# Performance work log

Hardware: AMD Instinct MI355X
Metric: run time of the kernel (lower is better)

The kernel has to match this reference:

```python
import jax, jax.numpy as jnp
import numpy as np

N_NODES = 50000
N_EDGES = 600000
IN_DIM = 64
HID = 128
LN_EPS = 1e-5


def setup_inputs() -> dict:
    key = jax.random.key(0)
    ks = jax.random.split(key, 10)
    x = jax.random.normal(ks[0], (N_NODES, IN_DIM), dtype=jnp.float32)
    edge_index = jax.random.randint(ks[1], (2, N_EDGES), 0, N_NODES, dtype=jnp.int64)
    def lin(k, fan_in, fan_out):
        bound = 1.0 / np.sqrt(fan_in)
        kw, kb = jax.random.split(k)
        W = jax.random.uniform(kw, (fan_in, fan_out), minval=-bound, maxval=bound, dtype=jnp.float32)
        b = jax.random.uniform(kb, (fan_out,), minval=-bound, maxval=bound, dtype=jnp.float32)
        return W, b
    W1, b1 = lin(ks[2], IN_DIM, HID)
    W2, b2 = lin(ks[3], HID, HID)
    W3, b3 = lin(ks[4], HID, HID)
    g1 = jnp.ones((HID,), jnp.float32); be1 = jnp.zeros((HID,), jnp.float32)
    g2 = jnp.ones((HID,), jnp.float32); be2 = jnp.zeros((HID,), jnp.float32)
    g3 = jnp.ones((HID,), jnp.float32); be3 = jnp.zeros((HID,), jnp.float32)
    return dict(x=x, edge_index=edge_index, W1=W1, b1=b1, W2=W2, b2=b2, W3=W3, b3=b3,
                g1=g1, be1=be1, g2=g2, be2=be2, g3=g3, be3=be3)


def _gnn_layer(h, W, b, src, dst, inv_cnt, g, be):
    # linear transform then mean aggregation over {neighbors ∪ self} (self-loops in src/dst)
    h = h @ W + b                                   # [N, HID]
    s = jax.ops.segment_sum(h[src], dst, num_segments=N_NODES)  # gather + scatter-sum
    h = s * inv_cnt                                 # mean aggregation
    h = jax.nn.relu(h)
    mu = jnp.mean(h, axis=-1, keepdims=True)
    var = jnp.var(h, axis=-1, keepdims=True)
    return g * (h - mu) * jax.lax.rsqrt(var + LN_EPS) + be


def reference(x, edge_index, W1, b1, W2, b2, W3, b3, g1, be1, g2, be2, g3, be3):
    loops = jnp.arange(N_NODES, dtype=edge_index.dtype)
    src = jnp.concatenate([edge_index[0], loops])   # message source (x_j)
    dst = jnp.concatenate([edge_index[1], loops])   # aggregation target
    cnt = jax.ops.segment_sum(jnp.ones_like(dst, dtype=x.dtype), dst, num_segments=N_NODES)
    inv_cnt = (1.0 / cnt)[:, None]                  # cnt >= 1 due to self loops
    h = _gnn_layer(x, W1, b1, src, dst, inv_cnt, g1, be1)
    h = _gnn_layer(h, W2, b2, src, dst, inv_cnt, g2, be2)
    h = _gnn_layer(h, W3, b3, src, dst, inv_cnt, g3, be3)
    return h
```

## Files before the change

### kernel.cpp

```cpp
#include <hip/hip_runtime.h>
#include <hip/hip_bf16.h>

#define N_NODES 50000
#define N_EDGES 600000
#define HID 128
#define LN_EPS 1e-5f

#define SCAN_BLOCK 1024
#define SCAN_NBLK ((N_NODES + SCAN_BLOCK - 1) / SCAN_BLOCK)

typedef __attribute__((ext_vector_type(8))) short bf16x8;
typedef __attribute__((ext_vector_type(4))) float f32x4;

static __device__ __forceinline__ unsigned short f2bf(float f) {
    union { float f; unsigned u; } v; v.f = f;
    unsigned u = v.u;
    u += 0x7fffu + ((u >> 16) & 1u);
    return (unsigned short)(u >> 16);
}
static __device__ __forceinline__ float bflo(unsigned u) {
    union { unsigned u; float f; } c; c.u = u << 16; return c.f;
}
static __device__ __forceinline__ float bfhi(unsigned u) {
    union { unsigned u; float f; } c; c.u = u & 0xffff0000u; return c.f;
}

__global__ __launch_bounds__(256) void count_kernel(const int* __restrict__ ei,
                                                    int* __restrict__ deg, int E) {
    int i = blockIdx.x * blockDim.x + threadIdx.x;
    if (i < E) atomicAdd(&deg[ei[E + i]], 1);
}

__global__ __launch_bounds__(SCAN_BLOCK) void deg_partial_kernel(const int* __restrict__ deg,
                                                                 int* __restrict__ partials, int n) {
    int t = threadIdx.x;
    int i = blockIdx.x * SCAN_BLOCK + t;
    int v = (i < n) ? deg[i] : 0;
    int s = v;
#pragma unroll
    for (int off = 1; off < 64; off <<= 1) s += __shfl_xor(s, off);
    __shared__ int ws[SCAN_BLOCK / 64];
    if ((t & 63) == 0) ws[t >> 6] = s;
    __syncthreads();
    if (t == 0) {
        int tot = 0;
#pragma unroll
        for (int w = 0; w < SCAN_BLOCK / 64; ++w) tot += ws[w];
        partials[blockIdx.x] = tot;
    }
}

__global__ __launch_bounds__(64) void scan_partials_kernel(int* __restrict__ partials,
                                                           int* __restrict__ row_ptr, int nblk) {
    int lane = threadIdx.x;
    int v = (lane < nblk) ? partials[lane] : 0;
    int incl = v;
#pragma unroll
    for (int off = 1; off < 64; off <<= 1) {
        int x = __shfl_up(incl, off);
        if (lane >= off) incl += x;
    }
    if (lane < nblk) partials[lane] = incl - v;
    if (lane == 63) row_ptr[N_NODES] = incl;
}

__global__ __launch_bounds__(SCAN_BLOCK) void scan_final_kernel(const int* __restrict__ deg,
                                                                const int* __restrict__ partials,
                                                                int* __restrict__ row_ptr,
                                                                int* __restrict__ cursor,
                                                                float* __restrict__ inv_cnt, int n) {
    int t = threadIdx.x;
    int i = blockIdx.x * SCAN_BLOCK + t;
    int v = (i < n) ? deg[i] : 0;
    int lane = t & 63, wid = t >> 6;
    int incl = v;
#pragma unroll
    for (int off = 1; off < 64; off <<= 1) {
        int x = __shfl_up(incl, off);
        if (lane >= off) incl += x;
    }
    __shared__ int ws[SCAN_BLOCK / 64];
    if (lane == 63) ws[wid] = incl;
    __syncthreads();
    int woff = 0;
    for (int w = 0; w < wid; ++w) woff += ws[w];
    int excl = partials[blockIdx.x] + woff + (incl - v);
    if (i < n) {
        row_ptr[i] = excl;
        cursor[i]  = excl;
        inv_cnt[i] = 1.0f / (float)(v + 1);
    }
}

__global__ __launch_bounds__(256) void fill_kernel(const int* __restrict__ ei,
                                                   int* __restrict__ cursor,
                                                   int* __restrict__ col, int E) {
    int i = blockIdx.x * blockDim.x + threadIdx.x;
    if (i < E) {
        int s = ei[i];
        int d = ei[E + i];
        int p = atomicAdd(&cursor[d], 1);
        col[p] = s;
    }
}

__global__ __launch_bounds__(256) void cast_x_kernel(const float* __restrict__ x,
                                                     unsigned short* __restrict__ xb, int n8) {
    int i = blockIdx.x * 256 + threadIdx.x;
    if (i < n8) {
        float4 a = ((const float4*)x)[i * 2];
        float4 b = ((const float4*)x)[i * 2 + 1];
        int4 o;
        o.x = (int)f2bf(a.x) | ((int)f2bf(a.y) << 16);
        o.y = (int)f2bf(a.z) | ((int)f2bf(a.w) << 16);
        o.z = (int)f2bf(b.x) | ((int)f2bf(b.y) << 16);
        o.w = (int)f2bf(b.z) | ((int)f2bf(b.w) << 16);
        ((int4*)xb)[i] = o;
    }
}

__global__ __launch_bounds__(256) void wswz_kernel(const float* __restrict__ W,
                                                   unsigned short* __restrict__ dst, int K) {
    int i = blockIdx.x * 256 + threadIdx.x;
    if (i < K * 128) {
        int k = i >> 7, col = i & 127;
        dst[(((k >> 3) * 128) + col) * 8 + (k & 7)] = f2bf(W[i]);
    }
}

template <int K>
__global__ __launch_bounds__(256) void gemm_mfma_kernel(
    const unsigned short* __restrict__ A,
    const unsigned short* __restrict__ Wswz,
    const float* __restrict__ bias,
    unsigned short* __restrict__ out, int N) {
    __shared__ unsigned short Bl[K * 128];
    __shared__ float bl[128];
    int t = threadIdx.x;
    for (int i = t; i < K * 16; i += 256)
        ((int4*)Bl)[i] = ((const int4*)Wswz)[i];
    if (t < 128) bl[t] = bias[t];
    __syncthreads();

    int lane = t & 63;
    int w = t >> 6;
    int r0 = blockIdx.x * 64 + w * 16;
    int colb = lane & 15;
    int kg = lane >> 4;
    int rowa = min(r0 + colb, N - 1);

    f32x4 acc[8];
#pragma unroll
    for (int c = 0; c < 8; ++c) acc[c] = (f32x4){0.f, 0.f, 0.f, 0.f};

    const bf16x8* Blv = (const bf16x8*)Bl;
    for (int s = 0; s < K; s += 32) {
        bf16x8 afrag = *(const bf16x8*)&A[(size_t)rowa * K + s + kg * 8];
        int kb = (s >> 3) + kg;
#pragma unroll
        for (int c = 0; c < 8; ++c) {
            bf16x8 bfrag = Blv[kb * 128 + c * 16 + colb];
            acc[c] = __builtin_amdgcn_mfma_f32_16x16x32_bf16(afrag, bfrag, acc[c], 0, 0, 0);
        }
    }
#pragma unroll
    for (int c = 0; c < 8; ++c) {
        int col = c * 16 + colb;
        float bv = bl[col];
#pragma unroll
        for (int r = 0; r < 4; ++r) {
            int ro = r0 + kg * 4 + r;
            if (ro < N) out[(size_t)ro * 128 + col] = f2bf(acc[c][r] + bv);
        }
    }
}

template <int BF16OUT>
__global__ __launch_bounds__(256) void agg_norm_kernel(
    const unsigned short* __restrict__ hb,
    const int* __restrict__ row_ptr,
    const int* __restrict__ col,
    const float* __restrict__ inv_cnt,
    const float* __restrict__ g, const float* __restrict__ be,
    void* __restrict__ outp, int N) {
    int tid  = blockIdx.x * 256 + threadIdx.x;
    int wave = tid >> 6;
    int lane = threadIdx.x & 63;
    int sub  = lane >> 4;
    int lc   = lane & 15;
    int n    = wave * 4 + sub;
    bool act = n < N;
    int nc   = act ? n : N - 1;

    const uint4* h4 = (const uint4*)hb;

    float a[8];
    {
        uint4 u = h4[(size_t)nc * 16 + lc];
        a[0] = bflo(u.x); a[1] = bfhi(u.x);
        a[2] = bflo(u.y); a[3] = bfhi(u.y);
        a[4] = bflo(u.z); a[5] = bfhi(u.z);
        a[6] = bflo(u.w); a[7] = bfhi(u.w);
    }

    int beg = row_ptr[nc], end = row_ptr[nc + 1];
    int cnt = end - beg;
    int lim = min(cnt, 32);
    int c0 = (lc < cnt)      ? col[beg + lc]      : nc;
    int c1 = (16 + lc < cnt) ? col[beg + 16 + lc] : nc;

    int wlim = lim;
    wlim = max(wlim, __shfl_xor(wlim, 16));
    wlim = max(wlim, __shfl_xor(wlim, 32));
    int nGrp = (wlim + 3) >> 2;

    for (int gi = 0; gi < nGrp; ++gi) {
        int e0 = gi * 4;
        int jj[4]; float mm[4];
#pragma unroll
        for (int q = 0; q < 4; ++q) {
            int iq = max(min(e0 + q, lim - 1), 0);
            mm[q] = (e0 + q < lim) ? 1.0f : 0.0f;
            int sl = sub * 16 + (iq & 15);
            int jA = __shfl(c0, sl);
            int jB = __shfl(c1, sl);
            jj[q] = (iq < 16) ? jA : jB;
        }
        uint4 u0 = h4[(size_t)jj[0] * 16 + lc];
        uint4 u1 = h4[(size_t)jj[1] * 16 + lc];
        uint4 u2 = h4[(size_t)jj[2] * 16 + lc];
        uint4 u3 = h4[(size_t)jj[3] * 16 + lc];
#define ACC(U, M)                                                              \
        a[0] = fmaf(M, bflo(U.x), a[0]); a[1] = fmaf(M, bfhi(U.x), a[1]);      \
        a[2] = fmaf(M, bflo(U.y), a[2]); a[3] = fmaf(M, bfhi(U.y), a[3]);      \
        a[4] = fmaf(M, bflo(U.z), a[4]); a[5] = fmaf(M, bfhi(U.z), a[5]);      \
        a[6] = fmaf(M, bflo(U.w), a[6]); a[7] = fmaf(M, bfhi(U.w), a[7]);
        ACC(u0, mm[0]) ACC(u1, mm[1]) ACC(u2, mm[2]) ACC(u3, mm[3])
#undef ACC
    }
    for (int e = 32; e < cnt; ++e) {
        int j = col[beg + e];
        uint4 u = h4[(size_t)j * 16 + lc];
        a[0] += bflo(u.x); a[1] += bfhi(u.x);
        a[2] += bflo(u.y); a[3] += bfhi(u.y);
        a[4] += bflo(u.z); a[5] += bfhi(u.z);
        a[6] += bflo(u.w); a[7] += bfhi(u.w);
    }

    float ic = inv_cnt[nc];
    float s[8], sum = 0.f, sq = 0.f;
#pragma unroll
    for (int k = 0; k < 8; ++k) {
        s[k] = fmaxf(a[k] * ic, 0.0f);
        sum += s[k];
        sq  += s[k] * s[k];
    }
#pragma unroll
    for (int off = 1; off < 16; off <<= 1) {
        sum += __shfl_xor(sum, off);
        sq  += __shfl_xor(sq, off);
    }
    float mu  = sum * (1.0f / 128.0f);
    float var = sq * (1.0f / 128.0f) - mu * mu;
    float rs  = rsqrtf(var + LN_EPS);

    const float4* gv  = (const float4*)g;
    const float4* bv  = (const float4*)be;
    float4 gA = gv[lc * 2], gB = gv[lc * 2 + 1];
    float4 bA = bv[lc * 2], bB = bv[lc * 2 + 1];
    float o[8];
    o[0] = gA.x * (s[0] - mu) * rs + bA.x;
    o[1] = gA.y * (s[1] - mu) * rs + bA.y;
    o[2] = gA.z * (s[2] - mu) * rs + bA.z;
    o[3] = gA.w * (s[3] - mu) * rs + bA.w;
    o[4] = gB.x * (s[4] - mu) * rs + bB.x;
    o[5] = gB.y * (s[5] - mu) * rs + bB.y;
    o[6] = gB.z * (s[6] - mu) * rs + bB.z;
    o[7] = gB.w * (s[7] - mu) * rs + bB.w;

    if (!act) return;
    if (BF16OUT) {
        uint4 p;
        p.x = (unsigned)f2bf(o[0]) | ((unsigned)f2bf(o[1]) << 16);
        p.y = (unsigned)f2bf(o[2]) | ((unsigned)f2bf(o[3]) << 16);
        p.z = (unsigned)f2bf(o[4]) | ((unsigned)f2bf(o[5]) << 16);
        p.w = (unsigned)f2bf(o[6]) | ((unsigned)f2bf(o[7]) << 16);
        ((uint4*)outp)[(size_t)n * 16 + lc] = p;
    } else {
        float4 f0; f0.x = o[0]; f0.y = o[1]; f0.z = o[2]; f0.w = o[3];
        float4 f1; f1.x = o[4]; f1.y = o[5]; f1.z = o[6]; f1.w = o[7];
        ((float4*)outp)[(size_t)n * 32 + lc * 2]     = f0;
        ((float4*)outp)[(size_t)n * 32 + lc * 2 + 1] = f1;
    }
}

extern "C" void kernel_launch(void* const* d_in, const int* in_sizes, int n_in,
                              void* d_out, int out_size, void* d_ws, size_t ws_size,
                              hipStream_t stream) {
    const float* x  = (const float*)d_in[0];
    const int*   ei = (const int*)d_in[1];
    const float* W1 = (const float*)d_in[2];
    const float* b1 = (const float*)d_in[3];
    const float* W2 = (const float*)d_in[4];
    const float* b2 = (const float*)d_in[5];
    const float* W3 = (const float*)d_in[6];
    const float* b3 = (const float*)d_in[7];
    const float* g1 = (const float*)d_in[8];
    const float* be1 = (const float*)d_in[9];
    const float* g2 = (const float*)d_in[10];
    const float* be2 = (const float*)d_in[11];
    const float* g3 = (const float*)d_in[12];
    const float* be3 = (const float*)d_in[13];
    float* out = (float*)d_out;

    const int N = N_NODES, E = N_EDGES;
    char* w = (char*)d_ws;
    unsigned short* hb   = (unsigned short*)w; w += (size_t)N * 128 * 2;
    unsigned short* midb = (unsigned short*)w; w += (size_t)N * 128 * 2;
    unsigned short* xb   = (unsigned short*)w; w += (size_t)N * 64 * 2;
    unsigned short* w1s  = (unsigned short*)w; w += (size_t)64 * 128 * 2;
    unsigned short* w2s  = (unsigned short*)w; w += (size_t)128 * 128 * 2;
    unsigned short* w3s  = (unsigned short*)w; w += (size_t)128 * 128 * 2;
    int*   col    = (int*)w;    w += (size_t)E * sizeof(int);
    int*   rowp   = (int*)w;    w += (size_t)(N + 1) * sizeof(int);
    int*   cursor = (int*)w;    w += (size_t)N * sizeof(int);
    int*   deg    = (int*)w;    w += (size_t)N * sizeof(int);
    float* invc   = (float*)w;  w += (size_t)N * sizeof(float);
    int*   parts  = (int*)w;    w += (size_t)SCAN_NBLK * sizeof(int);

    hipMemsetAsync(deg, 0, (size_t)N * sizeof(int), stream);
    count_kernel<<<(E + 255) / 256, 256, 0, stream>>>(ei, deg, E);
    deg_partial_kernel<<<SCAN_NBLK, SCAN_BLOCK, 0, stream>>>(deg, parts, N);
    scan_partials_kernel<<<1, 64, 0, stream>>>(parts, rowp, SCAN_NBLK);
    scan_final_kernel<<<SCAN_NBLK, SCAN_BLOCK, 0, stream>>>(deg, parts, rowp, cursor, invc, N);
    fill_kernel<<<(E + 255) / 256, 256, 0, stream>>>(ei, cursor, col, E);

    const int n8 = N * 64 / 8;
    cast_x_kernel<<<(n8 + 255) / 256, 256, 0, stream>>>(x, xb, n8);
    wswz_kernel<<<(64 * 128 + 255) / 256, 256, 0, stream>>>(W1, w1s, 64);
    wswz_kernel<<<(128 * 128 + 255) / 256, 256, 0, stream>>>(W2, w2s, 128);
    wswz_kernel<<<(128 * 128 + 255) / 256, 256, 0, stream>>>(W3, w3s, 128);

    const int gemm_blocks = (N + 63) / 64;
    const int agg_blocks  = (N + 15) / 16;

    gemm_mfma_kernel<64><<<gemm_blocks, 256, 0, stream>>>(xb, w1s, b1, hb, N);
    agg_norm_kernel<1><<<agg_blocks, 256, 0, stream>>>(hb, rowp, col, invc, g1, be1, midb, N);
    gemm_mfma_kernel<128><<<gemm_blocks, 256, 0, stream>>>(midb, w2s, b2, hb, N);
    agg_norm_kernel<1><<<agg_blocks, 256, 0, stream>>>(hb, rowp, col, invc, g2, be2, midb, N);
    gemm_mfma_kernel<128><<<gemm_blocks, 256, 0, stream>>>(midb, w3s, b3, hb, N);
    agg_norm_kernel<0><<<agg_blocks, 256, 0, stream>>>(hb, rowp, col, invc, g3, be3, out, N);
}
```

Before: 195.5 us.

## Sort nodes by degree for aggregation and widen gather batches to eight

```diff
diff --git a/kernel.cpp b/kernel.cpp
--- a/kernel.cpp
+++ b/kernel.cpp
@@ -101,6 +101,37 @@
         int d = ei[E + i];
         int p = atomicAdd(&cursor[d], 1);
         col[p] = s;
+    }
+}
+
+__global__ __launch_bounds__(256) void degsort_hist_kernel(const int* __restrict__ deg,
+                                                           int* __restrict__ bins, int n) {
+    int i = blockIdx.x * 256 + threadIdx.x;
+    if (i < n) atomicAdd(&bins[min(deg[i], 63)], 1);
+}
+
+__global__ __launch_bounds__(64) void degsort_scan_kernel(const int* __restrict__ bins,
+                                                          int* __restrict__ binoff) {
+    int lane = threadIdx.x;
+    int v = bins[lane];
+    int incl = v;
+#pragma unroll
+    for (int off = 1; off < 64; off <<= 1) {
+        int x = __shfl_up(incl, off);
+        if (lane >= off) incl += x;
+    }
+    binoff[lane] = incl - v;
+}
+
+__global__ __launch_bounds__(256) void degsort_place_kernel(const int* __restrict__ deg,
+                                                            const int* __restrict__ binoff,
+                                                            int* __restrict__ bcur,
+                                                            int* __restrict__ perm, int n) {
+    int i = blockIdx.x * 256 + threadIdx.x;
+    if (i < n) {
+        int b = min(deg[i], 63);
+        int p = atomicAdd(&bcur[b], 1);
+        perm[binoff[b] + p] = i;
     }
 }
 
@@ -181,6 +212,7 @@
     const int* __restrict__ row_ptr,
     const int* __restrict__ col,
     const float* __restrict__ inv_cnt,
+    const int* __restrict__ perm,
     const float* __restrict__ g, const float* __restrict__ be,
     void* __restrict__ outp, int N) {
     int tid  = blockIdx.x * 256 + threadIdx.x;
@@ -188,9 +220,9 @@
     int lane = threadIdx.x & 63;
     int sub  = lane >> 4;
     int lc   = lane & 15;
-    int n    = wave * 4 + sub;
-    bool act = n < N;
-    int nc   = act ? n : N - 1;
+    int idx  = wave * 4 + sub;
+    bool act = idx < N;
+    int nc   = act ? perm[idx] : 0;
 
     const uint4* h4 = (const uint4*)hb;
 
@@ -212,13 +244,13 @@
     int wlim = lim;
     wlim = max(wlim, __shfl_xor(wlim, 16));
     wlim = max(wlim, __shfl_xor(wlim, 32));
-    int nGrp = (wlim + 3) >> 2;
+    int nGrp = (wlim + 7) >> 3;
 
     for (int gi = 0; gi < nGrp; ++gi) {
-        int e0 = gi * 4;
-        int jj[4]; float mm[4];
-#pragma unroll
-        for (int q = 0; q < 4; ++q) {
+        int e0 = gi * 8;
+        int jj[8]; float mm[8];
+#pragma unroll
+        for (int q = 0; q < 8; ++q) {
             int iq = max(min(e0 + q, lim - 1), 0);
             mm[q] = (e0 + q < lim) ? 1.0f : 0.0f;
             int sl = sub * 16 + (iq & 15);
@@ -226,17 +258,16 @@
             int jB = __shfl(c1, sl);
             jj[q] = (iq < 16) ? jA : jB;
         }
-        uint4 u0 = h4[(size_t)jj[0] * 16 + lc];
-        uint4 u1 = h4[(size_t)jj[1] * 16 + lc];
-        uint4 u2 = h4[(size_t)jj[2] * 16 + lc];
-        uint4 u3 = h4[(size_t)jj[3] * 16 + lc];
-#define ACC(U, M)                                                              \
-        a[0] = fmaf(M, bflo(U.x), a[0]); a[1] = fmaf(M, bfhi(U.x), a[1]);      \
-        a[2] = fmaf(M, bflo(U.y), a[2]); a[3] = fmaf(M, bfhi(U.y), a[3]);      \
-        a[4] = fmaf(M, bflo(U.z), a[4]); a[5] = fmaf(M, bfhi(U.z), a[5]);      \
-        a[6] = fmaf(M, bflo(U.w), a[6]); a[7] = fmaf(M, bfhi(U.w), a[7]);
-        ACC(u0, mm[0]) ACC(u1, mm[1]) ACC(u2, mm[2]) ACC(u3, mm[3])
-#undef ACC
+        uint4 u[8];
+#pragma unroll
+        for (int q = 0; q < 8; ++q) u[q] = h4[(size_t)jj[q] * 16 + lc];
+#pragma unroll
+        for (int q = 0; q < 8; ++q) {
+            a[0] = fmaf(mm[q], bflo(u[q].x), a[0]); a[1] = fmaf(mm[q], bfhi(u[q].x), a[1]);
+            a[2] = fmaf(mm[q], bflo(u[q].y), a[2]); a[3] = fmaf(mm[q], bfhi(u[q].y), a[3]);
+            a[4] = fmaf(mm[q], bflo(u[q].z), a[4]); a[5] = fmaf(mm[q], bfhi(u[q].z), a[5]);
+            a[6] = fmaf(mm[q], bflo(u[q].w), a[6]); a[7] = fmaf(mm[q], bfhi(u[q].w), a[7]);
+        }
     }
     for (int e = 32; e < cnt; ++e) {
         int j = col[beg + e];
@@ -285,12 +316,12 @@
         p.y = (unsigned)f2bf(o[2]) | ((unsigned)f2bf(o[3]) << 16);
         p.z = (unsigned)f2bf(o[4]) | ((unsigned)f2bf(o[5]) << 16);
         p.w = (unsigned)f2bf(o[6]) | ((unsigned)f2bf(o[7]) << 16);
-        ((uint4*)outp)[(size_t)n * 16 + lc] = p;
+        ((uint4*)outp)[(size_t)nc * 16 + lc] = p;
     } else {
         float4 f0; f0.x = o[0]; f0.y = o[1]; f0.z = o[2]; f0.w = o[3];
         float4 f1; f1.x = o[4]; f1.y = o[5]; f1.z = o[6]; f1.w = o[7];
-        ((float4*)outp)[(size_t)n * 32 + lc * 2]     = f0;
-        ((float4*)outp)[(size_t)n * 32 + lc * 2 + 1] = f1;
+        ((float4*)outp)[(size_t)nc * 32 + lc * 2]     = f0;
+        ((float4*)outp)[(size_t)nc * 32 + lc * 2 + 1] = f1;
     }
 }
 
@@ -325,16 +356,24 @@
     int*   rowp   = (int*)w;    w += (size_t)(N + 1) * sizeof(int);
     int*   cursor = (int*)w;    w += (size_t)N * sizeof(int);
     int*   deg    = (int*)w;    w += (size_t)N * sizeof(int);
+    int*   bins   = (int*)w;    w += 64 * sizeof(int);
+    int*   bcur   = (int*)w;    w += 64 * sizeof(int);
+    int*   binoff = (int*)w;    w += 64 * sizeof(int);
+    int*   perm   = (int*)w;    w += (size_t)N * sizeof(int);
     float* invc   = (float*)w;  w += (size_t)N * sizeof(float);
     int*   parts  = (int*)w;    w += (size_t)SCAN_NBLK * sizeof(int);
 
-    hipMemsetAsync(deg, 0, (size_t)N * sizeof(int), stream);
+    hipMemsetAsync(deg, 0, ((size_t)N + 128) * sizeof(int), stream);
     count_kernel<<<(E + 255) / 256, 256, 0, stream>>>(ei, deg, E);
     deg_partial_kernel<<<SCAN_NBLK, SCAN_BLOCK, 0, stream>>>(deg, parts, N);
     scan_partials_kernel<<<1, 64, 0, stream>>>(parts, rowp, SCAN_NBLK);
     scan_final_kernel<<<SCAN_NBLK, SCAN_BLOCK, 0, stream>>>(deg, parts, rowp, cursor, invc, N);
     fill_kernel<<<(E + 255) / 256, 256, 0, stream>>>(ei, cursor, col, E);
 
+    degsort_hist_kernel<<<(N + 255) / 256, 256, 0, stream>>>(deg, bins, N);
+    degsort_scan_kernel<<<1, 64, 0, stream>>>(bins, binoff);
+    degsort_place_kernel<<<(N + 255) / 256, 256, 0, stream>>>(deg, binoff, bcur, perm, N);
+
     const int n8 = N * 64 / 8;
     cast_x_kernel<<<(n8 + 255) / 256, 256, 0, stream>>>(x, xb, n8);
     wswz_kernel<<<(64 * 128 + 255) / 256, 256, 0, stream>>>(W1, w1s, 64);
@@ -345,9 +384,9 @@
     const int agg_blocks  = (N + 15) / 16;
 
     gemm_mfma_kernel<64><<<gemm_blocks, 256, 0, stream>>>(xb, w1s, b1, hb, N);
-    agg_norm_kernel<1><<<agg_blocks, 256, 0, stream>>>(hb, rowp, col, invc, g1, be1, midb, N);
+    agg_norm_kernel<1><<<agg_blocks, 256, 0, stream>>>(hb, rowp, col, invc, perm, g1, be1, midb, N);
     gemm_mfma_kernel<128><<<gemm_blocks, 256, 0, stream>>>(midb, w2s, b2, hb, N);
-    agg_norm_kernel<1><<<agg_blocks, 256, 0, stream>>>(hb, rowp, col, invc, g2, be2, midb, N);
+    agg_norm_kernel<1><<<agg_blocks, 256, 0, stream>>>(hb, rowp, col, invc, perm, g2, be2, midb, N);
     gemm_mfma_kernel<128><<<gemm_blocks, 256, 0, stream>>>(midb, w3s, b3, hb, N);
-    agg_norm_kernel<0><<<agg_blocks, 256, 0, stream>>>(hb, rowp, col, invc, g3, be3, out, N);
-}
+    agg_norm_kernel<0><<<agg_blocks, 256, 0, stream>>>(hb, rowp, col, invc, perm, g3, be3, out, N);
+}
```

New measurement: 500.2 us. 2.56x slower.
